# Performance work log

Hardware: AMD Instinct MI355X
Metric: run time of the kernel (lower is better)

The kernel has to match this reference:

```python
import jax, jax.numpy as jnp
import numpy as np

NN_SIZE = 10          # k for kNN (includes the point itself as its own nearest neighbor)
COS_EPS = 1e-8        # torch.nn.CosineSimilarity eps


def _pairwise_sqdist(p):
    # p: (B,N,3) -> (B,N,N) squared euclidean distances without (B,N,N,3) intermediate
    x2 = jnp.sum(p * p, axis=-1)                      # (B,N)
    inner = jnp.einsum('bnd,bmd->bnm', p, p)          # (B,N,N)
    return x2[:, :, None] + x2[:, None, :] - 2.0 * inner


def _batch_normals(points):
    # points: (B,N,3) -> PCA normals (B,N,3)
    d = _pairwise_sqdist(points)                      # (B,N,N)
    _, idx = jax.lax.top_k(-d, NN_SIZE)               # (B,N,K) indices of k nearest
    nbrs = jax.vmap(lambda p, i: p[i])(points, idx)   # (B,N,K,3) gathered neighborhoods
    centered = nbrs - jnp.mean(nbrs, axis=2, keepdims=True)
    cov = jnp.einsum('bnki,bnkj->bnij', centered, centered) / NN_SIZE  # (B,N,3,3)
    _, vecs = jnp.linalg.eigh(cov)                    # eigenvalues ascending
    return vecs[..., :, 0]                            # eigvec of smallest eigval = normal


def setup_inputs() -> dict:
    key = jax.random.key(0)
    k1, k2 = jax.random.split(key)
    pred = jax.random.normal(k1, (8, 4096, 3), dtype=jnp.float32)
    gt_normals = jax.random.normal(k2, (8, 4096, 3), dtype=jnp.float32)
    return {"pred": pred, "gt_normals": gt_normals}


def reference(pred, gt_normals):
    pred_normals = _batch_normals(pred)                         # (B,N,3)
    dot = jnp.sum(pred_normals * gt_normals, axis=-1)           # (B,N)
    na = jnp.linalg.norm(pred_normals, axis=-1)
    nb = jnp.linalg.norm(gt_normals, axis=-1)
    cos = dot / (jnp.maximum(na, COS_EPS) * jnp.maximum(nb, COS_EPS))
    return jnp.mean(1.0 - cos)
```

## Files before the change

kernel.cpp:

```cpp
#include <hip/hip_runtime.h>
#include <math.h>


#define NPTS   4096
#define KNN    10
#define NBINS  256
#define XLO    (-5.5f)
#define INVBW  (256.0f / 11.0f)
#define W      1024
#define QPB    32
#define NB     1024
#define LISTCAP 32768

__device__ __forceinline__ unsigned int umed3(unsigned int a, unsigned int b, unsigned int c) {
    unsigned int r;
    asm("v_med3_u32 %0, %1, %2, %3" : "=v"(r) : "v"(a), "v"(b), "v"(c));
    return r;
}

__device__ __forceinline__ void sift(unsigned int nd[KNN], unsigned int key) {
#pragma unroll
    for (int t = KNN - 1; t >= 1; --t)
        nd[t] = umed3(key, nd[t - 1], nd[t]);
    nd[0] = nd[0] < key ? nd[0] : key;
}

__device__ __forceinline__ int xbin(float x) {
    int bin = (int)floorf((x - XLO) * INVBW);
    return bin < 0 ? 0 : (bin > NBINS - 1 ? NBINS - 1 : bin);
}

#define MAKE_KEY(q, c, J)                                                     \
    ({                                                                        \
        float sw_ = (q).w + (c).w;                                            \
        float dp_ = fmaf((q).x, (c).x, fmaf((q).y, (c).y, (q).z * (c).z));    \
        float d_  = fmaf(-2.0f, dp_, sw_);                                    \
        d_ = fmaxf(d_, 0.0f);                                                 \
        (__float_as_uint(d_) & 0xFFFFF000u) | (unsigned)(J);                  \
    })

__device__ float normal_loss3(const float nbx[KNN], const float nby[KNN],
                              const float nbz[KNN], const float* g3)
{
    float sx = 0.f, sy = 0.f, sz = 0.f;
#pragma unroll
    for (int t = 0; t < KNN; ++t) { sx += nbx[t]; sy += nby[t]; sz += nbz[t]; }
    float mx = sx / 10.0f, my = sy / 10.0f, mz = sz / 10.0f;
    float c00 = 0.f, c01 = 0.f, c02 = 0.f, c11 = 0.f, c12 = 0.f, c22 = 0.f;
#pragma unroll
    for (int t = 0; t < KNN; ++t) {
        float ux = nbx[t] - mx, uy = nby[t] - my, uz = nbz[t] - mz;
        c00 = fmaf(ux, ux, c00);
        c01 = fmaf(ux, uy, c01);
        c02 = fmaf(ux, uz, c02);
        c11 = fmaf(uy, uy, c11);
        c12 = fmaf(uy, uz, c12);
        c22 = fmaf(uz, uz, c22);
    }
    double a00 = (double)(c00 / 10.0f), a01 = (double)(c01 / 10.0f);
    double a02 = (double)(c02 / 10.0f), a11 = (double)(c11 / 10.0f);
    double a12 = (double)(c12 / 10.0f), a22 = (double)(c22 / 10.0f);

    double vx = 1.0, vy = 0.0, vz = 0.0;
    double qd = (a00 + a11 + a22) / 3.0;
    double p1 = a01 * a01 + a02 * a02 + a12 * a12;
    double b00 = a00 - qd, b11 = a11 - qd, b22 = a22 - qd;
    double p2 = b00 * b00 + b11 * b11 + b22 * b22 + 2.0 * p1;
    if (p2 > 1e-300) {
        double p = sqrt(p2 / 6.0);
        double inv = 1.0 / p;
        double m00 = b00 * inv, m01 = a01 * inv, m02 = a02 * inv;
        double m11 = b11 * inv, m12 = a12 * inv, m22 = b22 * inv;
        double detB = m00 * (m11 * m22 - m12 * m12)
                    - m01 * (m01 * m22 - m12 * m02)
                    + m02 * (m01 * m12 - m11 * m02);
        double r = 0.5 * detB;
        r = r < -1.0 ? -1.0 : (r > 1.0 ? 1.0 : r);
        double phi = acos(r) / 3.0;
        double eig0 = qd + 2.0 * p * cos(phi + 2.0943951023931953);
        double r0x = a00 - eig0, r0y = a01, r0z = a02;
        double r1y = a11 - eig0, r1z = a12;
        double r2z = a22 - eig0;
        double c0x = r0y * r1z - r0z * r1y;
        double c0y = r0z * r0y - r0x * r1z;
        double c0z = r0x * r1y - r0y * r0y;
        double c1x = r0y * r2z - r0z * r1z;
        double c1y = r0z * r0z - r0x * r2z;
        double c1z = r0x * r1z - r0y * r0z;
        double c2x = r1y * r2z - r1z * r1z;
        double c2y = r1z * r0z - r0y * r2z;
        double c2z = r0y * r1z - r1y * r0z;
        double n0 = c0x * c0x + c0y * c0y + c0z * c0z;
        double n1 = c1x * c1x + c1y * c1y + c1z * c1z;
        double n2 = c2x * c2x + c2y * c2y + c2z * c2z;
        double bx, by, bz, bn;
        if (n0 >= n1 && n0 >= n2) { bx = c0x; by = c0y; bz = c0z; bn = n0; }
        else if (n1 >= n2)        { bx = c1x; by = c1y; bz = c1z; bn = n1; }
        else                      { bx = c2x; by = c2y; bz = c2z; bn = n2; }
        if (bn > 1e-300) {
            double s = 1.0 / sqrt(bn);
            vx = bx * s; vy = by * s; vz = bz * s;
        }
    }
    float nx = (float)vx, ny = (float)vy, nz = (float)vz;
    float gx = g3[0], gy = g3[1], gz = g3[2];
    float dotg = nx * gx + ny * gy + nz * gz;
    float na = sqrtf(nx * nx + ny * ny + nz * nz);
    float gn = sqrtf(gx * gx + gy * gy + gz * gz);
    float cs = dotg / (fmaxf(na, 1e-8f) * fmaxf(gn, 1e-8f));
    return 1.0f - cs;
}

__global__ __launch_bounds__(1024) void gtnl_bin(
    const float* __restrict__ pred, float4* __restrict__ wsPts,
    unsigned int* __restrict__ wsCnt)
{
    __shared__ unsigned int hist[NBINS];
    __shared__ unsigned int bst[NBINS + 1];

    const int tid = threadIdx.x;
    const int b   = blockIdx.x;
    if (b == 0 && tid == 0) wsCnt[0] = 0;
    const float* src = pred + (size_t)b * NPTS * 3;

    if (tid < NBINS) hist[tid] = 0;
    __syncthreads();

    float px[4], py[4], pz[4];
    int   pb[4], pidx[4];
#pragma unroll
    for (int k = 0; k < 4; ++k) {
        int p = tid + 1024 * k;
        float x = src[3 * p + 0];
        float y = src[3 * p + 1];
        float z = src[3 * p + 2];
        int bin = xbin(x);
        px[k] = x; py[k] = y; pz[k] = z; pb[k] = bin; pidx[k] = p;
        atomicAdd(&hist[bin], 1u);
    }
    __syncthreads();

    if (tid < 64) {
        unsigned s0 = hist[4 * tid + 0], s1 = hist[4 * tid + 1];
        unsigned s2 = hist[4 * tid + 2], s3 = hist[4 * tid + 3];
        unsigned tot = s0 + s1 + s2 + s3;
        unsigned pre = tot;
#pragma unroll
        for (int d = 1; d < 64; d <<= 1) {
            unsigned t = __shfl_up(pre, d, 64);
            if (tid >= d) pre += t;
        }
        unsigned ex = pre - tot;
        bst[4 * tid + 0] = ex;
        bst[4 * tid + 1] = ex + s0;
        bst[4 * tid + 2] = ex + s0 + s1;
        bst[4 * tid + 3] = ex + s0 + s1 + s2;
        if (tid == 63) bst[NBINS] = ex + tot;
    }
    __syncthreads();

    if (tid < NBINS) hist[tid] = bst[tid];
    __syncthreads();

#pragma unroll
    for (int k = 0; k < 4; ++k) {
        unsigned pos = atomicAdd(&hist[pb[k]], 1u);
        wsPts[(size_t)b * NPTS + pos] =
            make_float4(px[k], py[k], pz[k], __uint_as_float((unsigned)pidx[k]));
    }
}

__global__ __launch_bounds__(256, 4) void gtnl_scan(
    const float4* __restrict__ wsPts, const float* __restrict__ gt,
    float* __restrict__ qloss, unsigned int* __restrict__ wsCnt,
    unsigned int* __restrict__ wsList)
{
    __shared__ float4 pts[W];
    __shared__ unsigned int mbuf[7][QPB][KNN];

    const int tid   = threadIdx.x;
    const int bid   = blockIdx.x;
    const int b     = bid >> 7;
    const int chunk = bid & 127;
    const int qbase = chunk * QPB;
    const int s     = tid >> 5;
    const int ql    = tid & 31;

    int W0 = qbase + QPB / 2 - W / 2;
    W0 = W0 < 0 ? 0 : (W0 > NPTS - W ? NPTS - W : W0);

    const float4* wp = wsPts + (size_t)b * NPTS;
    for (int i = tid; i < W; i += 256) {
        float4 v = wp[W0 + i];
        pts[i] = make_float4(v.x, v.y, v.z, fmaf(v.x, v.x, fmaf(v.y, v.y, v.z * v.z)));
    }
    __syncthreads();

    const int qpos = qbase + ql;
    const float4 q = pts[qpos - W0];

    unsigned int nd[KNN];
#pragma unroll
    for (int t = 0; t < KNN; ++t) nd[t] = 0x7F000000u;

#pragma unroll 8
    for (int t = 0; t < W / 8; ++t) {
        int j = 8 * t + s;
        float4 c = pts[j];
        sift(nd, MAKE_KEY(q, c, j));
    }

    if (s != 0) {
#pragma unroll
        for (int t = 0; t < KNN; ++t) mbuf[s - 1][ql][t] = nd[t];
    }
    __syncthreads();
    if (s != 0) return;

#pragma unroll
    for (int m = 0; m < 7; ++m)
#pragma unroll
        for (int t = 0; t < KNN; ++t) sift(nd, mbuf[m][ql][t]);

    unsigned int thr_bits = (nd[KNN - 1] & 0xFFFFF000u) + 0x1000u;
    float thr = __uint_as_float(thr_bits);
    float hw  = __uint_as_float(__float_as_uint(sqrtf(thr)) + 4) + 1e-3f;
    bool okL = (W0 == 0)        || (q.x - hw > pts[0].x);
    bool okR = (W0 == NPTS - W) || (q.x + hw < pts[W - 1].x);

    const unsigned int qorig = __float_as_uint(wp[qpos].w);
    float res = 0.0f;
    if (okL && okR) {
        float nbx[KNN], nby[KNN], nbz[KNN];
#pragma unroll
        for (int t = 0; t < KNN; ++t) {
            float4 pn = pts[nd[t] & 0xFFFu];
            nbx[t] = pn.x; nby[t] = pn.y; nbz[t] = pn.z;
        }
        res = normal_loss3(nbx, nby, nbz, gt + ((size_t)b * NPTS + qorig) * 3);
    } else {
        unsigned int idx = atomicAdd(wsCnt, 1u);
        wsList[idx] = ((unsigned)b << 12) | (unsigned)qpos;
    }
    qloss[(size_t)b * NPTS + qorig] = res;
}

__global__ __launch_bounds__(256, 4) void gtnl_fix(
    const float4* __restrict__ wsPts, const float* __restrict__ gt,
    float* __restrict__ qloss, const unsigned int* __restrict__ wsCnt,
    const unsigned int* __restrict__ wsList)
{
    const int lane = threadIdx.x & 63;
    const int wid  = blockIdx.x * 4 + (threadIdx.x >> 6);
    unsigned int n = wsCnt[0];

    for (unsigned int i = wid; i < n; i += 4096) {
        unsigned int e = wsList[i];
        const int b    = e >> 12;
        const int qpos = e & 0xFFF;
        const float4* wp = wsPts + (size_t)b * NPTS;

        float4 qv = wp[qpos];
        float4 q  = make_float4(qv.x, qv.y, qv.z,
                                fmaf(qv.x, qv.x, fmaf(qv.y, qv.y, qv.z * qv.z)));
        const unsigned int qorig = __float_as_uint(qv.w);

        unsigned int nd[KNN];
#pragma unroll
        for (int t = 0; t < KNN; ++t) nd[t] = 0x7F000000u;

#pragma unroll 8
        for (int t = 0; t < NPTS / 64; ++t) {
            int j = 64 * t + lane;
            float4 v = wp[j];
            float4 c = make_float4(v.x, v.y, v.z,
                                   fmaf(v.x, v.x, fmaf(v.y, v.y, v.z * v.z)));
            sift(nd, MAKE_KEY(q, c, j));
        }

        unsigned int keys[KNN];
#pragma unroll
        for (int r = 0; r < KNN; ++r) {
            unsigned int m = nd[0];
#pragma unroll
            for (int d = 1; d < 64; d <<= 1) {
                unsigned int o = __shfl_xor(m, d, 64);
                m = m < o ? m : o;
            }
            keys[r] = m;
            bool win = (nd[0] == m);
#pragma unroll
            for (int t = 0; t < KNN - 1; ++t) nd[t] = win ? nd[t + 1] : nd[t];
            nd[KNN - 1] = win ? 0xFFFFFFFFu : nd[KNN - 1];
        }

        float nbx[KNN], nby[KNN], nbz[KNN];
#pragma unroll
        for (int t = 0; t < KNN; ++t) {
            float4 pn = wp[keys[t] & 0xFFFu];
            nbx[t] = pn.x; nby[t] = pn.y; nbz[t] = pn.z;
        }
        float res = normal_loss3(nbx, nby, nbz, gt + ((size_t)b * NPTS + qorig) * 3);
        if (lane == 0) qloss[(size_t)b * NPTS + qorig] = res;
    }
}

__global__ __launch_bounds__(1024) void gtnl_reduceQ(
    const float* __restrict__ qloss, float* __restrict__ out)
{
    __shared__ float sbuf[1024];
    const int tid = threadIdx.x;
    const float4* q4 = (const float4*)qloss;
    float s = 0.0f;
#pragma unroll
    for (int t = 0; t < 8; ++t) {
        float4 v = q4[tid + 1024 * t];
        s += (v.x + v.y) + (v.z + v.w);
    }
    sbuf[tid] = s;
    __syncthreads();
    for (int k = 512; k > 0; k >>= 1) {
        if (tid < k) sbuf[tid] += sbuf[tid + k];
        __syncthreads();
    }
    if (tid == 0) out[0] = sbuf[0] / 32768.0f;
}

__global__ __launch_bounds__(256) void gtnl_brute(
    const float* __restrict__ pred, const float* __restrict__ gt,
    float* __restrict__ partial)
{
    __shared__ float4 ptsB[NPTS];
    __shared__ unsigned int mbuf[64][3][KNN];

    const int tid = threadIdx.x;
    const int b   = blockIdx.x >> 6;
    const int qc  = blockIdx.x & 63;
    const int ql  = tid & 63;
    const int sub = tid >> 6;
    const int qi  = qc * 64 + ql;

    const float* src = pred + (size_t)b * NPTS * 3;
    for (int p = tid; p < NPTS; p += 256) {
        float x = src[3 * p + 0], y = src[3 * p + 1], z = src[3 * p + 2];
        ptsB[p] = make_float4(x, y, z, fmaf(x, x, fmaf(y, y, z * z)));
    }
    __syncthreads();

    const float4 q = ptsB[qi];
    unsigned int nd[KNN];
#pragma unroll
    for (int t = 0; t < KNN; ++t) nd[t] = 0xFFFFFFFFu;

    const int j0 = sub * 1024;
#pragma unroll 8
    for (int j = j0; j < j0 + 1024; ++j) {
        float4 c = ptsB[j];
        sift(nd, MAKE_KEY(q, c, j));
    }

    if (sub != 0) {
#pragma unroll
        for (int t = 0; t < KNN; ++t) mbuf[ql][sub - 1][t] = nd[t];
    }
    __syncthreads();

    float res = 0.0f;
    if (sub == 0) {
#pragma unroll
        for (int ss = 0; ss < 3; ++ss)
#pragma unroll
            for (int t = 0; t < KNN; ++t) sift(nd, mbuf[ql][ss][t]);
        float nbx[KNN], nby[KNN], nbz[KNN];
#pragma unroll
        for (int t = 0; t < KNN; ++t) {
            float4 pn = ptsB[nd[t] & 0xFFFu];
            nbx[t] = pn.x; nby[t] = pn.y; nbz[t] = pn.z;
        }
        res = normal_loss3(nbx, nby, nbz, gt + ((size_t)b * NPTS + qi) * 3);
#pragma unroll
        for (int d = 32; d > 0; d >>= 1) res += __shfl_xor(res, d, 64);
    }
    __syncthreads();
    if (tid == 0) partial[blockIdx.x] = res;
}

__global__ __launch_bounds__(512) void gtnl_reduceP(
    const float* __restrict__ partial, float* __restrict__ out)
{
    __shared__ float sb[512];
    const int tid = threadIdx.x;
    sb[tid] = partial[tid];
    __syncthreads();
    for (int k = 256; k > 0; k >>= 1) {
        if (tid < k) sb[tid] += sb[tid + k];
        __syncthreads();
    }
    if (tid == 0) out[0] = sb[0] / 32768.0f;
}

extern "C" void kernel_launch(void* const* d_in, const int* in_sizes, int n_in,
                              void* d_out, int out_size, void* d_ws, size_t ws_size,
                              hipStream_t stream) {
    const float* pred = (const float*)d_in[0];
    const float* gt   = (const float*)d_in[1];
    float* out        = (float*)d_out;

    const size_t PTS_BYTES   = (size_t)8 * NPTS * sizeof(float4);
    const size_t QLOSS_BYTES = (size_t)8 * NPTS * sizeof(float);
    const size_t LIST_BYTES  = (size_t)LISTCAP * sizeof(unsigned);
    const size_t NEED = PTS_BYTES + QLOSS_BYTES + LIST_BYTES + 64;

    if (ws_size >= NEED) {
        float4*       wsPts  = (float4*)d_ws;
        float*        qloss  = (float*)((char*)d_ws + PTS_BYTES);
        unsigned int* wsList = (unsigned int*)((char*)d_ws + PTS_BYTES + QLOSS_BYTES);
        unsigned int* wsCnt  = (unsigned int*)((char*)d_ws + PTS_BYTES + QLOSS_BYTES + LIST_BYTES);

        gtnl_bin<<<8, 1024, 0, stream>>>(pred, wsPts, wsCnt);
        gtnl_scan<<<NB, 256, 0, stream>>>(wsPts, gt, qloss, wsCnt, wsList);
        gtnl_fix<<<NB, 256, 0, stream>>>(wsPts, gt, qloss, wsCnt, wsList);
        gtnl_reduceQ<<<1, 1024, 0, stream>>>(qloss, out);
    } else {
        float* partial = (float*)d_ws;
        gtnl_brute<<<512, 256, 0, stream>>>(pred, gt, partial);
        gtnl_reduceP<<<1, 512, 0, stream>>>(partial, out);
    }
}
```

Measured before the change: 62.76 us.

## Widen scan window, enlarge query blocks, fold final reduction into fix kernel

The scan kernel now uses a 1536-point window with 64 queries per block and 4 sub-slices per query, so fewer queries spill to the slow fix path and the per-query merge step shrinks. The separate reduction launch is removed: the last fix block, found with an atomic counter and threadfences, sums the per-query losses. This trades more per-thread scan work for fewer fallback queries and one less kernel launch, but halves the number of scan blocks, which may reduce occupancy.

```diff
diff --git a/kernel.cpp b/kernel.cpp
--- a/kernel.cpp
+++ b/kernel.cpp
@@ -7,9 +7,10 @@
 #define NBINS  256
 #define XLO    (-5.5f)
 #define INVBW  (256.0f / 11.0f)
-#define W      1024
-#define QPB    32
-#define NB     1024
+#define W      1536
+#define QPB    64
+#define NB     512
+#define FIXB   1024
 #define LISTCAP 32768
 
 __device__ __forceinline__ unsigned int umed3(unsigned int a, unsigned int b, unsigned int c) {
@@ -120,7 +121,7 @@
 
     const int tid = threadIdx.x;
     const int b   = blockIdx.x;
-    if (b == 0 && tid == 0) wsCnt[0] = 0;
+    if (b == 0 && tid < 2) wsCnt[tid] = 0;
     const float* src = pred + (size_t)b * NPTS * 3;
 
     if (tid < NBINS) hist[tid] = 0;
@@ -176,15 +177,15 @@
     unsigned int* __restrict__ wsList)
 {
     __shared__ float4 pts[W];
-    __shared__ unsigned int mbuf[7][QPB][KNN];
+    __shared__ unsigned int mbuf[3][QPB][KNN];
 
     const int tid   = threadIdx.x;
     const int bid   = blockIdx.x;
-    const int b     = bid >> 7;
-    const int chunk = bid & 127;
+    const int b     = bid >> 6;
+    const int chunk = bid & 63;
     const int qbase = chunk * QPB;
-    const int s     = tid >> 5;
-    const int ql    = tid & 31;
+    const int s     = tid >> 6;
+    const int ql    = tid & 63;
 
     int W0 = qbase + QPB / 2 - W / 2;
     W0 = W0 < 0 ? 0 : (W0 > NPTS - W ? NPTS - W : W0);
@@ -204,8 +205,8 @@
     for (int t = 0; t < KNN; ++t) nd[t] = 0x7F000000u;
 
 #pragma unroll 8
-    for (int t = 0; t < W / 8; ++t) {
-        int j = 8 * t + s;
+    for (int t = 0; t < W / 4; ++t) {
+        int j = 4 * t + s;
         float4 c = pts[j];
         sift(nd, MAKE_KEY(q, c, j));
     }
@@ -218,7 +219,7 @@
     if (s != 0) return;
 
 #pragma unroll
-    for (int m = 0; m < 7; ++m)
+    for (int m = 0; m < 3; ++m)
 #pragma unroll
         for (int t = 0; t < KNN; ++t) sift(nd, mbuf[m][ql][t]);
 
@@ -247,14 +248,16 @@
 
 __global__ __launch_bounds__(256, 4) void gtnl_fix(
     const float4* __restrict__ wsPts, const float* __restrict__ gt,
-    float* __restrict__ qloss, const unsigned int* __restrict__ wsCnt,
-    const unsigned int* __restrict__ wsList)
-{
-    const int lane = threadIdx.x & 63;
-    const int wid  = blockIdx.x * 4 + (threadIdx.x >> 6);
+    float* __restrict__ qloss, unsigned int* __restrict__ wsCnt,
+    const unsigned int* __restrict__ wsList, float* __restrict__ out)
+{
+    __shared__ float sbuf[256];
+    const int tid  = threadIdx.x;
+    const int lane = tid & 63;
+    const int wid  = blockIdx.x * 4 + (tid >> 6);
     unsigned int n = wsCnt[0];
 
-    for (unsigned int i = wid; i < n; i += 4096) {
+    for (unsigned int i = wid; i < n; i += FIXB * 4) {
         unsigned int e = wsList[i];
         const int b    = e >> 12;
         const int qpos = e & 0xFFF;
@@ -303,23 +306,24 @@
         float res = normal_loss3(nbx, nby, nbz, gt + ((size_t)b * NPTS + qorig) * 3);
         if (lane == 0) qloss[(size_t)b * NPTS + qorig] = res;
     }
-}
-
-__global__ __launch_bounds__(1024) void gtnl_reduceQ(
-    const float* __restrict__ qloss, float* __restrict__ out)
-{
-    __shared__ float sbuf[1024];
-    const int tid = threadIdx.x;
+
+    __threadfence();
+    __shared__ unsigned int isLast;
+    if (tid == 0) isLast = (atomicAdd(&wsCnt[1], 1u) == FIXB - 1) ? 1u : 0u;
+    __syncthreads();
+    if (!isLast) return;
+    __threadfence();
+
     const float4* q4 = (const float4*)qloss;
-    float s = 0.0f;
-#pragma unroll
-    for (int t = 0; t < 8; ++t) {
-        float4 v = q4[tid + 1024 * t];
-        s += (v.x + v.y) + (v.z + v.w);
-    }
-    sbuf[tid] = s;
-    __syncthreads();
-    for (int k = 512; k > 0; k >>= 1) {
+    float sum = 0.0f;
+#pragma unroll
+    for (int t = 0; t < 32; ++t) {
+        float4 v = q4[tid + 256 * t];
+        sum += (v.x + v.y) + (v.z + v.w);
+    }
+    sbuf[tid] = sum;
+    __syncthreads();
+    for (int k = 128; k > 0; k >>= 1) {
         if (tid < k) sbuf[tid] += sbuf[tid + k];
         __syncthreads();
     }
@@ -419,8 +423,7 @@
 
         gtnl_bin<<<8, 1024, 0, stream>>>(pred, wsPts, wsCnt);
         gtnl_scan<<<NB, 256, 0, stream>>>(wsPts, gt, qloss, wsCnt, wsList);
-        gtnl_fix<<<NB, 256, 0, stream>>>(wsPts, gt, qloss, wsCnt, wsList);
-        gtnl_reduceQ<<<1, 1024, 0, stream>>>(qloss, out);
+        gtnl_fix<<<FIXB, 256, 0, stream>>>(wsPts, gt, qloss, wsCnt, wsList, out);
     } else {
         float* partial = (float*)d_ws;
         gtnl_brute<<<512, 256, 0, stream>>>(pred, gt, partial);
```

Measured after the change: 112.2 us. 78.7% more time.
